# Performance work log

Hardware: AMD Instinct MI355X
Metric: run time of the kernel (lower is better)

The kernel has to match this reference:

```python
import jax, jax.numpy as jnp
import numpy as np

EPS = 1e-5


def setup_inputs() -> dict:
    key = jax.random.key(0)
    k1, k2, k3 = jax.random.split(key, 3)
    B, C, H, W = 4, 64, 512, 512
    x = jax.random.normal(k1, (B, C, H, W), dtype=jnp.float32)
    weight = jax.random.uniform(k2, (C,), dtype=jnp.float32, minval=0.5, maxval=1.5)
    bias = jax.random.normal(k3, (C,), dtype=jnp.float32) * 0.1
    return {"x": x, "weight": weight, "bias": bias}


def reference(x, weight, bias):
    # x: [B, C, H, W] -> BHWC rows, mask rows where any channel > 0,
    # BatchNorm1d (training-mode batch stats, biased var) over valid rows only,
    # scatter normalized rows back, untouched rows pass through.
    xb = jnp.transpose(x, (0, 2, 3, 1))            # [B, H, W, C]
    mask = jnp.any(xb > 0, axis=-1)                # [B, H, W]
    m = mask[..., None].astype(xb.dtype)           # [B, H, W, 1]
    count = jnp.maximum(jnp.sum(m), 1.0)           # number of valid rows
    mean = jnp.sum(xb * m, axis=(0, 1, 2)) / count             # [C]
    var = jnp.sum(jnp.square(xb - mean) * m, axis=(0, 1, 2)) / count  # [C] biased
    norm = (xb - mean) * jax.lax.rsqrt(var + EPS) * weight + bias
    out_bhwc = jnp.where(mask[..., None], norm, xb)
    return jnp.transpose(out_bhwc, (0, 3, 1, 2))   # [B, C, H, W]
```

## Files before the change

### kernel.cpp

```cpp
#include <hip/hip_runtime.h>
#include <cstdint>

#define BATCH 4
#define CH    64
#define HH    512
#define WW    512
#define HWSZ  (HH*WW)
#define NLOC  (BATCH*HWSZ)
#define NB_STATS (NLOC/256)
#define EPS_BN 1e-5f

__global__ __launch_bounds__(256) void stats_kernel(
    const float* __restrict__ x,
    float* __restrict__ psum,
    float* __restrict__ psumsq,
    float* __restrict__ pcount,
    unsigned char* __restrict__ maskout)
{
    const int tid = threadIdx.x;
    const int q   = tid >> 6;
    const int l   = tid & 63;
    const int loc_base = blockIdx.x * 256;
    const int b       = loc_base >> 18;
    const int hw_base = loc_base & (HWSZ - 1);
    const int cbase   = q * 16;

    __shared__ unsigned int pmw[4][64];
    __shared__ float slds [64][67];
    __shared__ float s2lds[64][67];
    __shared__ float comb[2][4][64];

    const float* xb = x + ((size_t)b * CH) * HWSZ + hw_base + l * 4;
    float4 val[16];
#pragma unroll
    for (int i = 0; i < 16; ++i)
        val[i] = *(const float4*)(xb + (size_t)(cbase + i) * HWSZ);

    unsigned int bits = 0;
#pragma unroll
    for (int i = 0; i < 16; ++i) {
        bits |= (val[i].x > 0.f ? 1u : 0u)
              | (val[i].y > 0.f ? 2u : 0u)
              | (val[i].z > 0.f ? 4u : 0u)
              | (val[i].w > 0.f ? 8u : 0u);
    }

    pmw[q][l] = bits;
    __syncthreads();
    const unsigned int allbits =
        pmw[0][l] | pmw[1][l] | pmw[2][l] | pmw[3][l];

    const float m0 = (allbits & 1u) ? 1.f : 0.f;
    const float m1 = (allbits & 2u) ? 1.f : 0.f;
    const float m2 = (allbits & 4u) ? 1.f : 0.f;
    const float m3 = (allbits & 8u) ? 1.f : 0.f;

    if (q == 0) {
        unsigned int packed = (allbits & 1u ? 1u : 0u)
                            | (allbits & 2u ? 0x100u : 0u)
                            | (allbits & 4u ? 0x10000u : 0u)
                            | (allbits & 8u ? 0x1000000u : 0u);
        *(unsigned int*)(maskout + loc_base + l * 4) = packed;

        float cnt = (float)__popc(allbits & 0xFu);
#pragma unroll
        for (int off = 32; off; off >>= 1)
            cnt += __shfl_xor(cnt, off, 64);
        if (l == 0) pcount[blockIdx.x] = cnt;
    }

#pragma unroll
    for (int i = 0; i < 16; ++i) {
        const float t0 = val[i].x * m0;
        const float t1 = val[i].y * m1;
        const float t2 = val[i].z * m2;
        const float t3 = val[i].w * m3;
        slds [cbase + i][l] = (t0 + t1) + (t2 + t3);
        s2lds[cbase + i][l] = (t0 * val[i].x + t1 * val[i].y)
                            + (t2 * val[i].z + t3 * val[i].w);
    }
    __syncthreads();

    {
        const int c    = tid & 63;
        const int part = tid >> 6;
        float s = 0.f, s2 = 0.f;
#pragma unroll
        for (int j = 0; j < 16; ++j) {
            s  += slds [c][part * 16 + j];
            s2 += s2lds[c][part * 16 + j];
        }
        comb[0][part][c] = s;
        comb[1][part][c] = s2;
    }
    __syncthreads();

    if (tid < 64) {
        const float fs  = (comb[0][0][tid] + comb[0][1][tid])
                        + (comb[0][2][tid] + comb[0][3][tid]);
        const float fs2 = (comb[1][0][tid] + comb[1][1][tid])
                        + (comb[1][2][tid] + comb[1][3][tid]);
        psum  [(size_t)blockIdx.x * 64 + tid] = fs;
        psumsq[(size_t)blockIdx.x * 64 + tid] = fs2;
    }
}

__global__ __launch_bounds__(256) void reduce_kernel(
    const float* __restrict__ psum,
    const float* __restrict__ psumsq,
    const float* __restrict__ pcount,
    const float* __restrict__ weight,
    const float* __restrict__ bias,
    float* __restrict__ scale,
    float* __restrict__ shift)
{
    const int c   = blockIdx.x;
    const int tid = threadIdx.x;
    float s = 0.f, s2 = 0.f, cn = 0.f;
    for (int i = tid; i < NB_STATS; i += 256) {
        s  += psum  [(size_t)i * 64 + c];
        s2 += psumsq[(size_t)i * 64 + c];
        cn += pcount[i];
    }
    __shared__ float ls[256], ls2[256], lc[256];
    ls[tid] = s; ls2[tid] = s2; lc[tid] = cn;
    __syncthreads();
#pragma unroll
    for (int off = 128; off; off >>= 1) {
        if (tid < off) {
            ls [tid] += ls [tid + off];
            ls2[tid] += ls2[tid + off];
            lc [tid] += lc [tid + off];
        }
        __syncthreads();
    }
    if (tid == 0) {
        const float cnt  = fmaxf(lc[0], 1.f);
        const float mean = ls[0] / cnt;
        const float var  = ls2[0] / cnt - mean * mean;
        const float inv  = rsqrtf(var + EPS_BN);
        const float wv   = weight[c];
        scale[c] = inv * wv;
        shift[c] = bias[c] - mean * inv * wv;
    }
}

__global__ __launch_bounds__(256) void norm_kernel(
    const float* __restrict__ x,
    const unsigned char* __restrict__ mask,
    const float* __restrict__ scale,
    const float* __restrict__ shift,
    float* __restrict__ out)
{
    const size_t t = (size_t)blockIdx.x * 256 + threadIdx.x;
    const size_t e = t * 4;
    const int c  = (int)((e >> 18) & 63);
    const int b  = (int)(e >> 24);
    const int hw = (int)(e & (HWSZ - 1));
    const int loc = (b << 18) | hw;

    const float4 v = *(const float4*)(x + e);
    const unsigned int mm = *(const unsigned int*)(mask + loc);
    const float sc = scale[c];
    const float sh = shift[c];

    float4 o;
    o.x = (mm & 0x000000FFu) ? fmaf(v.x, sc, sh) : v.x;
    o.y = (mm & 0x0000FF00u) ? fmaf(v.y, sc, sh) : v.y;
    o.z = (mm & 0x00FF0000u) ? fmaf(v.z, sc, sh) : v.z;
    o.w = (mm & 0xFF000000u) ? fmaf(v.w, sc, sh) : v.w;

    *(float4*)(out + e) = o;
}

extern "C" void kernel_launch(void* const* d_in, const int* in_sizes, int n_in,
                              void* d_out, int out_size, void* d_ws, size_t ws_size,
                              hipStream_t stream) {
    const float* x      = (const float*)d_in[0];
    const float* weight = (const float*)d_in[1];
    const float* bias   = (const float*)d_in[2];
    float* out = (float*)d_out;

    float* psum   = (float*)d_ws;
    float* psumsq = psum   + (size_t)NB_STATS * 64;
    float* pcount = psumsq + (size_t)NB_STATS * 64;
    float* scale  = pcount + NB_STATS;
    float* shift  = scale + 64;
    unsigned char* mask = (unsigned char*)(shift + 64);

    stats_kernel<<<NB_STATS, 256, 0, stream>>>(x, psum, psumsq, pcount, mask);
    reduce_kernel<<<CH, 256, 0, stream>>>(psum, psumsq, pcount, weight, bias,
                                          scale, shift);
    const int norm_blocks = (BATCH * CH * HWSZ) / 4 / 256;
    norm_kernel<<<norm_blocks, 256, 0, stream>>>(x, mask, scale, shift, out);
}
```

Measured before the change: 158.4 us.

## Replace partial-sum reduce kernel with global atomics and fold finalize into norm

The stats kernel now accumulates per-channel sums, sums of squares and the valid-row count straight into global totals with atomicAdd, instead of writing per-block partials. The separate reduce kernel is removed. Every norm thread now computes mean, variance, scale and shift from those totals, and a tiny zero kernel clears the accumulators first. This drops one kernel and the partial-sum round trip through memory, at the cost of heavy atomic contention on 129 addresses (4096 blocks × 64 channels), order-dependent float summation, and redundant per-thread rsqrt work.

```diff
diff --git a/kernel.cpp b/kernel.cpp
--- a/kernel.cpp
+++ b/kernel.cpp
@@ -3,18 +3,22 @@
 
 #define BATCH 4
 #define CH    64
-#define HH    512
-#define WW    512
-#define HWSZ  (HH*WW)
+#define HWSZ  262144
 #define NLOC  (BATCH*HWSZ)
 #define NB_STATS (NLOC/256)
+#define NORM_BLOCKS ((BATCH*CH*HWSZ)/4/256)
 #define EPS_BN 1e-5f
+
+__global__ void zero_kernel(float* __restrict__ g)
+{
+    if (threadIdx.x < 129) g[threadIdx.x] = 0.f;
+}
 
 __global__ __launch_bounds__(256) void stats_kernel(
     const float* __restrict__ x,
-    float* __restrict__ psum,
-    float* __restrict__ psumsq,
-    float* __restrict__ pcount,
+    float* __restrict__ gsum,
+    float* __restrict__ gsumsq,
+    float* __restrict__ gcount,
     unsigned char* __restrict__ maskout)
 {
     const int tid = threadIdx.x;
@@ -66,7 +70,7 @@
 #pragma unroll
         for (int off = 32; off; off >>= 1)
             cnt += __shfl_xor(cnt, off, 64);
-        if (l == 0) pcount[blockIdx.x] = cnt;
+        if (l == 0) atomicAdd(gcount, cnt);
     }
 
 #pragma unroll
@@ -100,56 +104,19 @@
                         + (comb[0][2][tid] + comb[0][3][tid]);
         const float fs2 = (comb[1][0][tid] + comb[1][1][tid])
                         + (comb[1][2][tid] + comb[1][3][tid]);
-        psum  [(size_t)blockIdx.x * 64 + tid] = fs;
-        psumsq[(size_t)blockIdx.x * 64 + tid] = fs2;
-    }
-}
-
-__global__ __launch_bounds__(256) void reduce_kernel(
-    const float* __restrict__ psum,
-    const float* __restrict__ psumsq,
-    const float* __restrict__ pcount,
-    const float* __restrict__ weight,
-    const float* __restrict__ bias,
-    float* __restrict__ scale,
-    float* __restrict__ shift)
-{
-    const int c   = blockIdx.x;
-    const int tid = threadIdx.x;
-    float s = 0.f, s2 = 0.f, cn = 0.f;
-    for (int i = tid; i < NB_STATS; i += 256) {
-        s  += psum  [(size_t)i * 64 + c];
-        s2 += psumsq[(size_t)i * 64 + c];
-        cn += pcount[i];
-    }
-    __shared__ float ls[256], ls2[256], lc[256];
-    ls[tid] = s; ls2[tid] = s2; lc[tid] = cn;
-    __syncthreads();
-#pragma unroll
-    for (int off = 128; off; off >>= 1) {
-        if (tid < off) {
-            ls [tid] += ls [tid + off];
-            ls2[tid] += ls2[tid + off];
-            lc [tid] += lc [tid + off];
-        }
-        __syncthreads();
-    }
-    if (tid == 0) {
-        const float cnt  = fmaxf(lc[0], 1.f);
-        const float mean = ls[0] / cnt;
-        const float var  = ls2[0] / cnt - mean * mean;
-        const float inv  = rsqrtf(var + EPS_BN);
-        const float wv   = weight[c];
-        scale[c] = inv * wv;
-        shift[c] = bias[c] - mean * inv * wv;
+        atomicAdd(&gsum  [tid], fs);
+        atomicAdd(&gsumsq[tid], fs2);
     }
 }
 
 __global__ __launch_bounds__(256) void norm_kernel(
     const float* __restrict__ x,
     const unsigned char* __restrict__ mask,
-    const float* __restrict__ scale,
-    const float* __restrict__ shift,
+    const float* __restrict__ gsum,
+    const float* __restrict__ gsumsq,
+    const float* __restrict__ gcount,
+    const float* __restrict__ weight,
+    const float* __restrict__ bias,
     float* __restrict__ out)
 {
     const size_t t = (size_t)blockIdx.x * 256 + threadIdx.x;
@@ -159,10 +126,15 @@
     const int hw = (int)(e & (HWSZ - 1));
     const int loc = (b << 18) | hw;
 
+    const float cnt  = fmaxf(gcount[0], 1.f);
+    const float mean = gsum[c] / cnt;
+    const float var  = gsumsq[c] / cnt - mean * mean;
+    const float inv  = rsqrtf(var + EPS_BN);
+    const float sc   = inv * weight[c];
+    const float sh   = bias[c] - mean * sc;
+
     const float4 v = *(const float4*)(x + e);
     const unsigned int mm = *(const unsigned int*)(mask + loc);
-    const float sc = scale[c];
-    const float sh = shift[c];
 
     float4 o;
     o.x = (mm & 0x000000FFu) ? fmaf(v.x, sc, sh) : v.x;
@@ -181,16 +153,13 @@
     const float* bias   = (const float*)d_in[2];
     float* out = (float*)d_out;
 
-    float* psum   = (float*)d_ws;
-    float* psumsq = psum   + (size_t)NB_STATS * 64;
-    float* pcount = psumsq + (size_t)NB_STATS * 64;
-    float* scale  = pcount + NB_STATS;
-    float* shift  = scale + 64;
-    unsigned char* mask = (unsigned char*)(shift + 64);
+    float* gsum   = (float*)d_ws;
+    float* gsumsq = gsum + 64;
+    float* gcount = gsumsq + 64;
+    unsigned char* mask = (unsigned char*)(gcount + 1);
 
-    stats_kernel<<<NB_STATS, 256, 0, stream>>>(x, psum, psumsq, pcount, mask);
-    reduce_kernel<<<CH, 256, 0, stream>>>(psum, psumsq, pcount, weight, bias,
-                                          scale, shift);
-    const int norm_blocks = (BATCH * CH * HWSZ) / 4 / 256;
-    norm_kernel<<<norm_blocks, 256, 0, stream>>>(x, mask, scale, shift, out);
+    zero_kernel<<<1, 256, 0, stream>>>(gsum);
+    stats_kernel<<<NB_STATS, 256, 0, stream>>>(x, gsum, gsumsq, gcount, mask);
+    norm_kernel<<<NORM_BLOCKS, 256, 0, stream>>>(x, mask, gsum, gsumsq, gcount,
+                                                 weight, bias, out);
 }
```

Measured after the change: 195.1 us. 23.1% more time.
